# Performance work log

Hardware: AMD Instinct MI355X
Metric: run time of the kernel (lower is better)

Reference implementation:

```python
import jax, jax.numpy as jnp
import numpy as np

NUM_EXPERTS = 8
D_MODEL = 1024
HIDDEN = 3 * D_MODEL
TOP_K = 2
LAMBDA = 0.01


def setup_inputs() -> dict:
    key = jax.random.key(0)
    k_x, k_w1, k_w2, k_r = jax.random.split(key, 4)
    B, T, C = 4, 2048, D_MODEL
    x = jax.random.normal(k_x, (B, T, C), dtype=jnp.float32)
    # per-expert SwishFFN weights (bias=False): W1 [E, C, H], W2 [E, H, C]
    W1 = jax.random.normal(k_w1, (NUM_EXPERTS, C, HIDDEN), dtype=jnp.float32) * (1.0 / np.sqrt(C))
    W2 = jax.random.normal(k_w2, (NUM_EXPERTS, HIDDEN, C), dtype=jnp.float32) * (1.0 / np.sqrt(HIDDEN))
    # router projection [C, E]
    Wr = jax.random.normal(k_r, (C, NUM_EXPERTS), dtype=jnp.float32) * (1.0 / np.sqrt(C))
    return {"x": x, "W1": W1, "W2": W2, "Wr": Wr}


def reference(x, W1, W2, Wr):
    B, T, C = x.shape
    E = W1.shape[0]
    xf = x.reshape(-1, C)                       # [N, C], N = B*T
    N = xf.shape[0]

    # Router: softmax over experts, keep top-k, renormalize among the k
    logits = xf @ Wr                            # [N, E]
    all_probs = jax.nn.softmax(logits, axis=-1)
    vals, idx = jax.lax.top_k(all_probs, TOP_K)  # [N, K]
    vals = vals / jnp.sum(vals, axis=-1, keepdims=True)
    routing_weight = jnp.zeros((N, E), dtype=xf.dtype).at[
        jnp.arange(N)[:, None], idx
    ].set(vals)                                  # sparse [N, E]

    # Expert combine: sum_e w_e * FFN_e(x); w_e == 0 for non-selected tokens,
    # so this equals the original masked gather/scatter loop exactly.
    out = jnp.zeros_like(xf)
    for e in range(E):
        h = jax.nn.silu(xf @ W1[e])              # [N, H]
        out = out + routing_weight[:, e:e + 1] * (h @ W2[e])

    # Load-balancing aux loss (fi detached)
    fi = jax.lax.stop_gradient(
        jnp.mean((routing_weight > 0).astype(xf.dtype), axis=0))
    pi = jnp.mean(all_probs, axis=0)
    aux_loss = LAMBDA * E * jnp.sum(fi * pi)

    return out.reshape(B, T, C), aux_loss
```

## Files before the change

kernel.cpp:

```cpp
#include <hip/hip_runtime.h>
#include <stdint.h>

#define N_TOK 8192
#define C_DIM 1024
#define H_DIM 3072
#define N_EXP 8
#define N_ASSIGN (N_TOK * 2)

typedef __attribute__((ext_vector_type(8))) short short8;
typedef __attribute__((ext_vector_type(4))) float f32x4;

__device__ __forceinline__ unsigned short f2bf(float f) {
    union { float f; uint32_t u; } v; v.f = f;
    uint32_t r = (v.u + 0x7FFFu + ((v.u >> 16) & 1u)) >> 16;
    return (unsigned short)r;
}

#define GLDS16(SRC, DST) __builtin_amdgcn_global_load_lds( \
    (const __attribute__((address_space(1))) void*)(SRC),  \
    (__attribute__((address_space(3))) void*)(DST), 16, 0, 0)

__global__ void transpose_bf16_kernel(const float* __restrict__ in, unsigned short* __restrict__ out,
                                      int rows, int cols) {
    __shared__ float tile[32][33];
    int e = blockIdx.z;
    const float* ip = in + (size_t)e * rows * cols;
    unsigned short* op = out + (size_t)e * rows * cols;
    int col0 = blockIdx.x * 32;
    int row0 = blockIdx.y * 32;
    int tx = threadIdx.x, ty = threadIdx.y;
    tile[ty][tx] = ip[(size_t)(row0 + ty) * cols + col0 + tx];
    __syncthreads();
    op[(size_t)(col0 + ty) * rows + row0 + tx] = f2bf(tile[tx][ty]);
}

__global__ __launch_bounds__(256) void router_kernel(const float* __restrict__ x, const float* __restrict__ Wr,
                                                     int2* __restrict__ idx2, float2* __restrict__ wgt2,
                                                     float* __restrict__ piAcc, int* __restrict__ cntAcc) {
    __shared__ float s_pi[8];
    __shared__ int s_cnt[8];
    int t = threadIdx.x;
    if (t < 8) { s_pi[t] = 0.f; s_cnt[t] = 0; }
    __syncthreads();
    int lane = t & 63;
    int wid = t >> 6;
    int gwv = blockIdx.x * 4 + wid;
    int nw = gridDim.x * 4;
    for (int n = gwv; n < N_TOK; n += nw) {
        float acc[8];
#pragma unroll
        for (int e = 0; e < 8; e++) acc[e] = 0.f;
        const float* xr = x + (size_t)n * C_DIM;
#pragma unroll
        for (int j = 0; j < 16; j++) {
            int k = lane + 64 * j;
            float xv = xr[k];
            const float4* wr4 = (const float4*)(Wr + (size_t)k * 8);
            float4 a = wr4[0], b = wr4[1];
            acc[0] += xv * a.x; acc[1] += xv * a.y; acc[2] += xv * a.z; acc[3] += xv * a.w;
            acc[4] += xv * b.x; acc[5] += xv * b.y; acc[6] += xv * b.z; acc[7] += xv * b.w;
        }
#pragma unroll
        for (int off = 1; off < 64; off <<= 1) {
#pragma unroll
            for (int e = 0; e < 8; e++) acc[e] += __shfl_xor(acc[e], off, 64);
        }
        float m = acc[0];
#pragma unroll
        for (int e = 1; e < 8; e++) m = fmaxf(m, acc[e]);
        float p[8]; float s = 0.f;
#pragma unroll
        for (int e = 0; e < 8; e++) { p[e] = __expf(acc[e] - m); s += p[e]; }
        float inv = 1.f / s;
#pragma unroll
        for (int e = 0; e < 8; e++) p[e] *= inv;
        int i0 = 0; float l0 = acc[0];
#pragma unroll
        for (int e = 1; e < 8; e++) if (acc[e] > l0) { l0 = acc[e]; i0 = e; }
        int i1 = -1; float l1 = -1e30f;
#pragma unroll
        for (int e = 0; e < 8; e++) if (e != i0 && acc[e] > l1) { l1 = acc[e]; i1 = e; }
        if (lane == 0) {
            float v0 = p[i0], v1 = p[i1];
            float rs = 1.f / (v0 + v1);
            idx2[n] = make_int2(i0, i1);
            wgt2[n] = make_float2(v0 * rs, v1 * rs);
            atomicAdd(&s_cnt[i0], 1);
            atomicAdd(&s_cnt[i1], 1);
#pragma unroll
            for (int e = 0; e < 8; e++) atomicAdd(&s_pi[e], p[e]);
        }
    }
    __syncthreads();
    if (t < 8) { atomicAdd(&piAcc[t], s_pi[t]); atomicAdd(&cntAcc[t], s_cnt[t]); }
}

__global__ void finalize_router_kernel(const int* __restrict__ cnt, const float* __restrict__ pi,
                                       int* __restrict__ off, float* __restrict__ aux_out) {
    if (threadIdx.x == 0) {
        int o = 0;
        float dot = 0.f;
        for (int e = 0; e < 8; e++) {
            off[e] = o;
            o += cnt[e];
            dot += (float)cnt[e] * pi[e];
        }
        aux_out[0] = 0.01f * 8.f * dot / ((float)N_TOK * (float)N_TOK);
    }
}

__global__ __launch_bounds__(256) void scatter_kernel(const int2* __restrict__ idx2, const float2* __restrict__ wgt2,
                                                      const int* __restrict__ off, int* __restrict__ cursor,
                                                      int* __restrict__ tok, float* __restrict__ gwArr) {
    __shared__ int lcnt[8], lbase[8];
    int t = threadIdx.x;
    if (t < 8) lcnt[t] = 0;
    __syncthreads();
    int a = blockIdx.x * 256 + t;
    int n = a >> 1, k = a & 1;
    int2 id = idx2[n];
    float2 w = wgt2[n];
    int e = k ? id.y : id.x;
    float wv = k ? w.y : w.x;
    int rank = atomicAdd(&lcnt[e], 1);
    __syncthreads();
    if (t < 8) lbase[t] = atomicAdd(&cursor[t], lcnt[t]);
    __syncthreads();
    int pos = off[e] + lbase[e] + rank;
    tok[pos] = n;
    gwArr[pos] = wv;
}

__global__ __launch_bounds__(256) void gather_kernel(const float* __restrict__ x, const int* __restrict__ tok,
                                                     unsigned short* __restrict__ xg) {
    int wid = threadIdx.x >> 6, lane = threadIdx.x & 63;
    int row = blockIdx.x * 4 + wid;
    int n = tok[row];
    const float4* src = (const float4*)(x + (size_t)n * C_DIM);
    ushort4* dst = (ushort4*)(xg + (size_t)row * C_DIM);
#pragma unroll
    for (int j = 0; j < 4; j++) {
        float4 v = src[lane + 64 * j];
        ushort4 o;
        o.x = f2bf(v.x); o.y = f2bf(v.y); o.z = f2bf(v.z); o.w = f2bf(v.w);
        dst[lane + 64 * j] = o;
    }
}

#define GEMM_BODY(WAITSTR, DOSTAGE)                                                 \
    {                                                                               \
        __builtin_amdgcn_sched_barrier(0);                                          \
        asm volatile(WAITSTR ::: "memory");                                         \
        __builtin_amdgcn_sched_barrier(0);                                          \
        __builtin_amdgcn_s_barrier();                                               \
        __builtin_amdgcn_sched_barrier(0);                                          \
        int bb = (t & 3) * 16384;                                                   \
        short8 a[8], b[4];                                                          \
        _Pragma("unroll")                                                           \
        for (int m = 0; m < 8; m++) a[m] = *(const short8*)&smem[bb + offA[m]];     \
        _Pragma("unroll")                                                           \
        for (int n = 0; n < 4; n++) b[n] = *(const short8*)&smem[bb + offB[n]];     \
        if (DOSTAGE) STAGE((t + 3) & 3);                                            \
        __builtin_amdgcn_s_setprio(1);                                              \
        _Pragma("unroll")                                                           \
        for (int m = 0; m < 8; m++)                                                 \
            _Pragma("unroll")                                                       \
            for (int n = 0; n < 4; n++)                                             \
                acc[m][n] = __builtin_amdgcn_mfma_f32_16x16x32_bf16(a[m], b[n], acc[m][n], 0, 0, 0); \
        __builtin_amdgcn_s_setprio(0);                                              \
    }

template <int EPI>
__global__ __launch_bounds__(512, 2) void moe_gemm_kernel(
    const unsigned short* __restrict__ A, int ldA,
    const unsigned short* __restrict__ Bt, int ldB, int bRowOff, int bColOff,
    int K,
    const int* __restrict__ cnt, const int* __restrict__ off,
    const int* __restrict__ tok, const float* __restrict__ gwArr,
    unsigned short* __restrict__ hs, int ldH,
    float* __restrict__ out) {
    __shared__ unsigned short smem[65536];
    const int MB = 16;
    int wg = blockIdx.x;
    int e = wg & 7;
    int loc = wg >> 3;
    int y = loc / MB;
    int mblk = loc - y * MB;
    int M = cnt[e];
    int m0 = mblk * 256;
    if (m0 >= M) return;
    int baseRow = off[e];
    int n0 = y * 256;
    int tid = threadIdx.x;
    int lane = tid & 63;
    int wid = tid >> 6;
    int wm = (wid >> 2) * 128;
    int wn = (wid & 3) * 64;

    f32x4 acc[8][4];
#pragma unroll
    for (int i = 0; i < 8; i++)
#pragma unroll
        for (int j = 0; j < 4; j++) acc[i][j] = (f32x4)0.f;

    const unsigned short* Bex = Bt + (size_t)e * (size_t)(C_DIM * H_DIM);

    const unsigned short* srcA[2];
    const unsigned short* srcB[2];
    int ldsOff[2];
#pragma unroll
    for (int i = 0; i < 2; i++) {
        int c = i * 512 + tid;
        int rl = c >> 3, cl = c & 7;
        int cls = cl ^ (rl & 7);
        int row = (rl << 1) | (cls >> 2);
        int kc = cls & 3;
        int rg = m0 + row; if (rg > M - 1) rg = M - 1;
        srcA[i] = A + (size_t)(baseRow + rg) * ldA + kc * 8;
        srcB[i] = Bex + (size_t)(bRowOff + n0 + row) * ldB + bColOff + kc * 8;
        ldsOff[i] = (c & ~63) * 8;
    }
    auto STAGE = [&](int buf) {
        int bb = buf * 16384;
#pragma unroll
        for (int i = 0; i < 2; i++) {
            GLDS16(srcA[i], &smem[bb + ldsOff[i]]);
            GLDS16(srcB[i], &smem[bb + 8192 + ldsOff[i]]);
            srcA[i] += 32; srcB[i] += 32;
        }
    };

    int kq = lane >> 4;
    int rsub = lane & 15;
    int offA[8], offB[4];
#pragma unroll
    for (int m = 0; m < 8; m++) {
        int r = wm + m * 16 + rsub;
        int rl = r >> 1;
        int cls = (((r & 1) << 2) | kq) ^ (rl & 7);
        offA[m] = rl * 64 + cls * 8;
    }
#pragma unroll
    for (int n = 0; n < 4; n++) {
        int r = wn + n * 16 + rsub;
        int rl = r >> 1;
        int cls = (((r & 1) << 2) | kq) ^ (rl & 7);
        offB[n] = 8192 + rl * 64 + cls * 8;
    }

    int nt = K >> 5;
    STAGE(0); STAGE(1); STAGE(2);
    int t = 0;
#pragma unroll 1
    for (; t < nt - 2; ++t) GEMM_BODY("s_waitcnt vmcnt(8)", (t + 3 < nt))
    GEMM_BODY("s_waitcnt vmcnt(4)", false); ++t;
    GEMM_BODY("s_waitcnt vmcnt(0)", false);

    int gRow = (lane >> 4) * 4;
    int cLane = lane & 15;
#pragma unroll
    for (int m = 0; m < 8; m++) {
#pragma unroll
        for (int j = 0; j < 4; j++) {
            int r = m0 + wm + m * 16 + gRow + j;
            if (r < M) {
                if (EPI == 0) {
#pragma unroll
                    for (int n = 0; n < 4; n++) {
                        int c = n0 + wn + n * 16 + cLane;
                        float v = acc[m][n][j];
                        float sv = v / (1.f + __expf(-v));
                        hs[(size_t)(baseRow + r) * ldH + c] = f2bf(sv);
                    }
                } else {
                    int token = tok[baseRow + r];
                    float w = gwArr[baseRow + r];
#pragma unroll
                    for (int n = 0; n < 4; n++) {
                        int c = n0 + wn + n * 16 + cLane;
                        atomicAdd(&out[(size_t)token * C_DIM + c], w * acc[m][n][j]);
                    }
                }
            }
        }
    }
}

extern "C" void kernel_launch(void* const* d_in, const int* in_sizes, int n_in,
                              void* d_out, int out_size, void* d_ws, size_t ws_size,
                              hipStream_t stream) {
    const float* x = (const float*)d_in[0];
    const float* W1 = (const float*)d_in[1];
    const float* W2 = (const float*)d_in[2];
    const float* Wr = (const float*)d_in[3];
    float* out = (float*)d_out;

    char* p = (char*)d_ws;
    auto alloc = [&](size_t bytes) {
        char* r = p;
        p += (bytes + 255) & ~(size_t)255;
        return r;
    };
    float* pi = (float*)alloc(8 * sizeof(float));
    int* cntA = (int*)alloc(8 * sizeof(int));
    int* cursor = (int*)alloc(8 * sizeof(int));
    int* offA = (int*)alloc(8 * sizeof(int));
    int2* idx2 = (int2*)alloc((size_t)N_TOK * sizeof(int2));
    float2* wgt2 = (float2*)alloc((size_t)N_TOK * sizeof(float2));
    int* tok = (int*)alloc((size_t)N_ASSIGN * sizeof(int));
    float* gwA = (float*)alloc((size_t)N_ASSIGN * sizeof(float));
    unsigned short* W1bT = (unsigned short*)alloc((size_t)N_EXP * C_DIM * H_DIM * 2);
    unsigned short* W2bT = (unsigned short*)alloc((size_t)N_EXP * C_DIM * H_DIM * 2);
    unsigned short* xg = (unsigned short*)alloc((size_t)N_ASSIGN * C_DIM * 2);
    size_t used = (size_t)(p - (char*)d_ws);
    size_t remain = ws_size > used ? ws_size - used : 0;
    int HC = H_DIM;
    while (HC > 384 && (size_t)N_ASSIGN * HC * 2 > remain) HC >>= 1;
    unsigned short* hs = (unsigned short*)p;

    hipMemsetAsync(d_ws, 0, 1024, stream);
    hipMemsetAsync(d_out, 0, (size_t)N_TOK * C_DIM * sizeof(float), stream);

    dim3 tb(32, 32, 1);
    transpose_bf16_kernel<<<dim3(H_DIM / 32, C_DIM / 32, N_EXP), tb, 0, stream>>>(W1, W1bT, C_DIM, H_DIM);
    transpose_bf16_kernel<<<dim3(C_DIM / 32, H_DIM / 32, N_EXP), tb, 0, stream>>>(W2, W2bT, H_DIM, C_DIM);

    router_kernel<<<256, 256, 0, stream>>>(x, Wr, idx2, wgt2, pi, cntA);
    finalize_router_kernel<<<1, 64, 0, stream>>>(cntA, pi, offA, out + (size_t)N_TOK * C_DIM);
    scatter_kernel<<<N_ASSIGN / 256, 256, 0, stream>>>(idx2, wgt2, offA, cursor, tok, gwA);
    gather_kernel<<<N_ASSIGN / 4, 256, 0, stream>>>(x, tok, xg);

    int nChunks = H_DIM / HC;
    for (int ci = 0; ci < nChunks; ++ci) {
        int h0 = ci * HC;
        int ny1 = HC / 256;
        moe_gemm_kernel<0><<<dim3(8 * ny1 * 16, 1, 1), 512, 0, stream>>>(
            xg, C_DIM, W1bT, C_DIM, h0, 0, C_DIM, cntA, offA, tok, gwA, hs, HC, out);
        moe_gemm_kernel<1><<<dim3(8 * 4 * 16, 1, 1), 512, 0, stream>>>(
            hs, HC, W2bT, H_DIM, 0, h0, HC, cntA, offA, tok, gwA, hs, HC, out);
    }
}
```

Baseline: 528.6 us.

## Split GEMM K-step into half-tiles with interleaved staging and compact grid

Rewrites the MFMA main loop so each K tile is processed in two halves of the M fragments, with the A and B global-to-LDS loads for future stages issued separately between them and barriers placed around each MFMA burst. The goal is to overlap LDS reads and global prefetch with matrix work and to keep register pressure lower. The grid also changes from a fixed 16 M-blocks per expert to a compact mapping that walks the expert counts, so no workgroups launch only to exit early. The extra barriers per tile add synchronisation cost, and the grid is sized at 72 blocks per N column, which could miss blocks if the routing is highly skewed.

```diff
diff --git a/kernel.cpp b/kernel.cpp
--- a/kernel.cpp
+++ b/kernel.cpp
@@ -147,50 +147,75 @@
     }
 }
 
-#define GEMM_BODY(WAITSTR, DOSTAGE)                                                 \
-    {                                                                               \
-        __builtin_amdgcn_sched_barrier(0);                                          \
-        asm volatile(WAITSTR ::: "memory");                                         \
-        __builtin_amdgcn_sched_barrier(0);                                          \
-        __builtin_amdgcn_s_barrier();                                               \
-        __builtin_amdgcn_sched_barrier(0);                                          \
-        int bb = (t & 3) * 16384;                                                   \
-        short8 a[8], b[4];                                                          \
-        _Pragma("unroll")                                                           \
-        for (int m = 0; m < 8; m++) a[m] = *(const short8*)&smem[bb + offA[m]];     \
-        _Pragma("unroll")                                                           \
-        for (int n = 0; n < 4; n++) b[n] = *(const short8*)&smem[bb + offB[n]];     \
-        if (DOSTAGE) STAGE((t + 3) & 3);                                            \
-        __builtin_amdgcn_s_setprio(1);                                              \
-        _Pragma("unroll")                                                           \
-        for (int m = 0; m < 8; m++)                                                 \
-            _Pragma("unroll")                                                       \
-            for (int n = 0; n < 4; n++)                                             \
-                acc[m][n] = __builtin_amdgcn_mfma_f32_16x16x32_bf16(a[m], b[n], acc[m][n], 0, 0, 0); \
-        __builtin_amdgcn_s_setprio(0);                                              \
+#define VM_WAIT(S) do { __builtin_amdgcn_sched_barrier(0);                   \
+    asm volatile(S ::: "memory");                                            \
+    __builtin_amdgcn_sched_barrier(0); } while (0)
+
+#define TILE_STEP(BB, SA, SB, WAITOP)                                        \
+    {                                                                        \
+        const unsigned short* Ab = &smem[(BB)];                              \
+        short8 aa[4], bb4[4];                                                \
+        _Pragma("unroll")                                                    \
+        for (int m = 0; m < 4; m++) aa[m] = *(const short8*)&Ab[offA[m]];    \
+        _Pragma("unroll")                                                    \
+        for (int n = 0; n < 4; n++) bb4[n] = *(const short8*)&Ab[offB[n]];   \
+        SA;                                                                  \
+        __builtin_amdgcn_s_barrier();                                        \
+        __builtin_amdgcn_sched_barrier(0);                                   \
+        __builtin_amdgcn_s_setprio(1);                                       \
+        _Pragma("unroll")                                                    \
+        for (int m = 0; m < 4; m++)                                          \
+            _Pragma("unroll")                                                \
+            for (int n = 0; n < 4; n++)                                      \
+                acc[m][n] = __builtin_amdgcn_mfma_f32_16x16x32_bf16(aa[m], bb4[n], acc[m][n], 0, 0, 0); \
+        __builtin_amdgcn_s_setprio(0);                                       \
+        __builtin_amdgcn_s_barrier();                                        \
+        __builtin_amdgcn_sched_barrier(0);                                   \
+        _Pragma("unroll")                                                    \
+        for (int m = 0; m < 4; m++) aa[m] = *(const short8*)&Ab[offA[4 + m]];\
+        SB;                                                                  \
+        WAITOP;                                                              \
+        __builtin_amdgcn_s_barrier();                                        \
+        __builtin_amdgcn_sched_barrier(0);                                   \
+        __builtin_amdgcn_s_setprio(1);                                       \
+        _Pragma("unroll")                                                    \
+        for (int m = 0; m < 4; m++)                                          \
+            _Pragma("unroll")                                                \
+            for (int n = 0; n < 4; n++)                                      \
+                acc[4 + m][n] = __builtin_amdgcn_mfma_f32_16x16x32_bf16(aa[m], bb4[n], acc[4 + m][n], 0, 0, 0); \
+        __builtin_amdgcn_s_setprio(0);                                       \
+        __builtin_amdgcn_s_barrier();                                        \
+        __builtin_amdgcn_sched_barrier(0);                                   \
     }
 
 template <int EPI>
 __global__ __launch_bounds__(512, 2) void moe_gemm_kernel(
     const unsigned short* __restrict__ A, int ldA,
     const unsigned short* __restrict__ Bt, int ldB, int bRowOff, int bColOff,
-    int K,
+    int K, int NY,
     const int* __restrict__ cnt, const int* __restrict__ off,
     const int* __restrict__ tok, const float* __restrict__ gwArr,
     unsigned short* __restrict__ hs, int ldH,
     float* __restrict__ out) {
     __shared__ unsigned short smem[65536];
-    const int MB = 16;
-    int wg = blockIdx.x;
-    int e = wg & 7;
-    int loc = wg >> 3;
-    int y = loc / MB;
-    int mblk = loc - y * MB;
+
+    int wi = blockIdx.x;
+    int base = 0, e = -1, enb = 0, local = 0;
+#pragma unroll
+    for (int i = 0; i < 8; i++) {
+        int nb = (cnt[i] + 255) >> 8;
+        int sz = nb * NY;
+        if (e < 0 && wi < base + sz) { e = i; enb = nb; local = wi - base; }
+        base += sz;
+    }
+    if (e < 0) return;
+    int y = local / enb;
+    int mblk = local - y * enb;
     int M = cnt[e];
     int m0 = mblk * 256;
-    if (m0 >= M) return;
     int baseRow = off[e];
     int n0 = y * 256;
+
     int tid = threadIdx.x;
     int lane = tid & 63;
     int wid = tid >> 6;
@@ -220,14 +245,17 @@
         srcB[i] = Bex + (size_t)(bRowOff + n0 + row) * ldB + bColOff + kc * 8;
         ldsOff[i] = (c & ~63) * 8;
     }
-    auto STAGE = [&](int buf) {
-        int bb = buf * 16384;
-#pragma unroll
-        for (int i = 0; i < 2; i++) {
-            GLDS16(srcA[i], &smem[bb + ldsOff[i]]);
-            GLDS16(srcB[i], &smem[bb + 8192 + ldsOff[i]]);
-            srcA[i] += 32; srcB[i] += 32;
-        }
+    auto STAGE_A = [&](int buf) {
+        int bbase = buf * 16384;
+        GLDS16(srcA[0], &smem[bbase + ldsOff[0]]);
+        GLDS16(srcA[1], &smem[bbase + ldsOff[1]]);
+        srcA[0] += 32; srcA[1] += 32;
+    };
+    auto STAGE_B = [&](int buf) {
+        int bbase = buf * 16384 + 8192;
+        GLDS16(srcB[0], &smem[bbase + ldsOff[0]]);
+        GLDS16(srcB[1], &smem[bbase + ldsOff[1]]);
+        srcB[0] += 32; srcB[1] += 32;
     };
 
     int kq = lane >> 4;
@@ -249,12 +277,20 @@
     }
 
     int nt = K >> 5;
-    STAGE(0); STAGE(1); STAGE(2);
-    int t = 0;
+    STAGE_A(0); STAGE_B(0); STAGE_A(1); STAGE_B(1); STAGE_A(2); STAGE_B(2);
+    VM_WAIT("s_waitcnt vmcnt(8)");
+    __builtin_amdgcn_s_barrier();
+    __builtin_amdgcn_sched_barrier(0);
+
+    int tt = 0;
 #pragma unroll 1
-    for (; t < nt - 2; ++t) GEMM_BODY("s_waitcnt vmcnt(8)", (t + 3 < nt))
-    GEMM_BODY("s_waitcnt vmcnt(4)", false); ++t;
-    GEMM_BODY("s_waitcnt vmcnt(0)", false);
+    for (; tt < nt - 3; ++tt) {
+        TILE_STEP((tt & 3) * 16384, STAGE_A((tt + 3) & 3), STAGE_B((tt + 3) & 3),
+                  VM_WAIT("s_waitcnt vmcnt(8)"))
+    }
+    TILE_STEP((tt & 3) * 16384, ((void)0), ((void)0), VM_WAIT("s_waitcnt vmcnt(4)")); ++tt;
+    TILE_STEP((tt & 3) * 16384, ((void)0), ((void)0), VM_WAIT("s_waitcnt vmcnt(0)")); ++tt;
+    TILE_STEP((tt & 3) * 16384, ((void)0), ((void)0), ((void)0));
 
     int gRow = (lane >> 4) * 4;
     int cLane = lane & 15;
@@ -334,9 +370,9 @@
     for (int ci = 0; ci < nChunks; ++ci) {
         int h0 = ci * HC;
         int ny1 = HC / 256;
-        moe_gemm_kernel<0><<<dim3(8 * ny1 * 16, 1, 1), 512, 0, stream>>>(
-            xg, C_DIM, W1bT, C_DIM, h0, 0, C_DIM, cntA, offA, tok, gwA, hs, HC, out);
-        moe_gemm_kernel<1><<<dim3(8 * 4 * 16, 1, 1), 512, 0, stream>>>(
-            hs, HC, W2bT, H_DIM, 0, h0, HC, cntA, offA, tok, gwA, hs, HC, out);
-    }
-}
+        moe_gemm_kernel<0><<<dim3(72 * ny1, 1, 1), 512, 0, stream>>>(
+            xg, C_DIM, W1bT, C_DIM, h0, 0, C_DIM, ny1, cntA, offA, tok, gwA, hs, HC, out);
+        moe_gemm_kernel<1><<<dim3(72 * 4, 1, 1), 512, 0, stream>>>(
+            hs, HC, W2bT, H_DIM, 0, h0, HC, 4, cntA, offA, tok, gwA, hs, HC, out);
+    }
+}
```

New measurement: 536.1 us. No clear change (+1.4%).
